# Kernel optimization log

Hardware: AMD Instinct MI355X
Metric: run time of the kernel (lower is better)

## Reference

```python
import jax, jax.numpy as jnp
import numpy as np

T, B, NIN, NOUT, H, NLAYER = 512, 32, 72, 90, 512, 5


def _ln(x, g, b):
    m = jnp.mean(x, -1, keepdims=True)
    v = jnp.var(x, -1, keepdims=True)
    return (x - m) * jax.lax.rsqrt(v + 1e-5) * g + b


def _sru_dir(xt, fp, rp, hw, vf, vr, bf, br):
    # xt/fp/rp/hw: (T, B, H) in scan order; elementwise gated recurrence
    def step(c, inp):
        x_t, f_t, r_t, hw_t = inp
        f = jax.nn.sigmoid(f_t + vf * c + bf)
        r = jax.nn.sigmoid(r_t + vr * c + br)
        c2 = f * c + (1.0 - f) * x_t
        h = r * jnp.tanh(c2) + (1.0 - r) * hw_t
        return c2, h
    c0 = jnp.zeros_like(xt[0])
    cT, hs = jax.lax.scan(step, c0, (xt, fp, rp, hw))
    return hs, cT


def _sru_layer(x, W, v, b, g, be, k):
    # x: (T, B, d_in); W: (d_in, 2*k*H); v,b: (2 dirs, 2 gates, H)
    Tl, Bl = x.shape[0], x.shape[1]
    xn = _ln(x, g, be)
    U = (xn @ W).reshape(Tl, Bl, 2, k, H)
    outs, cs = [], []
    for d in range(2):
        Ud = U[:, :, d]
        if d == 1:
            Ud = jnp.flip(Ud, 0)
        # highway: extra projection when d_in != H (k=4), else raw input (k=3)
        hw = Ud[:, :, 3] if k == 4 else (jnp.flip(x, 0) if d == 1 else x)
        hs, cT = _sru_dir(Ud[:, :, 0], Ud[:, :, 1], Ud[:, :, 2], hw,
                          v[d, 0], v[d, 1], b[d, 0], b[d, 1])
        if d == 1:
            hs = jnp.flip(hs, 0)
        outs.append(hs)
        cs.append(cT)
    return jnp.concatenate(outs, -1), jnp.concatenate(cs, -1)


def setup_inputs() -> dict:
    key = jax.random.key(0)
    ks = jax.random.split(key, 12)
    s1 = 1.0 / np.sqrt(NIN)
    s2 = 1.0 / np.sqrt(2 * H)
    s0 = 1.0 / np.sqrt(H)
    return {
        "x": jax.random.normal(ks[0], (T, B, NIN), jnp.float32),
        "W1": jax.random.normal(ks[1], (NIN, H), jnp.float32) * s1,
        "b1": jnp.zeros((H,), jnp.float32),
        "W2": jax.random.normal(ks[2], (2 * H, NOUT), jnp.float32) * s2,
        "b2": jnp.zeros((NOUT,), jnp.float32),
        # SRU layer 0: input H -> 2 dirs * H, k=3 (highway uses raw input)
        "W0": jax.random.normal(ks[3], (H, 2 * 3 * H), jnp.float32) * s0,
        "v0": jax.random.normal(ks[4], (2, 2, H), jnp.float32) * s0,
        "bb0": jnp.zeros((2, 2, H), jnp.float32),
        "g0": jnp.ones((H,), jnp.float32),
        "be0": jnp.zeros((H,), jnp.float32),
        # SRU layers 1..4: input 2H -> 2 dirs * H, k=4 (projected highway)
        "Ws": jax.random.normal(ks[5], (NLAYER - 1, 2 * H, 2 * 4 * H), jnp.float32) * s2,
        "vs": jax.random.normal(ks[6], (NLAYER - 1, 2, 2, H), jnp.float32) * s0,
        "bbs": jnp.zeros((NLAYER - 1, 2, 2, H), jnp.float32),
        "gs": jnp.ones((NLAYER - 1, 2 * H), jnp.float32),
        "bes": jnp.zeros((NLAYER - 1, 2 * H), jnp.float32),
    }


def reference(x, W1, b1, W2, b2, W0, v0, bb0, g0, be0, Ws, vs, bbs, gs, bes):
    h = jax.nn.relu(x @ W1 + b1)  # (T, B, H); dropout is identity at eval
    states = []
    h, c = _sru_layer(h, W0, v0, bb0, g0, be0, 3)
    states.append(c)
    for i in range(Ws.shape[0]):
        h, c = _sru_layer(h, Ws[i], vs[i], bbs[i], gs[i], bes[i], 4)
        states.append(c)
    out = h @ W2 + b2  # (T, B, NOUT)
    return out, jnp.stack(states)  # h state: (NLAYER, B, 2H)
```

## Files before the change

kernel.cpp:

```cpp
#include <hip/hip_runtime.h>
#include <stdint.h>

#define T_LEN 512
#define BATCH 32
#define NIN   72
#define NOUT  90
#define HDIM  512
#define MROWS (T_LEN*BATCH)

typedef unsigned short u16;
typedef unsigned int   u32;

typedef __bf16 bf16x8 __attribute__((ext_vector_type(8)));
typedef short  s16x8  __attribute__((ext_vector_type(8)));
typedef float  f32x4  __attribute__((ext_vector_type(4)));

__device__ __forceinline__ float b2f(u16 u){ return __uint_as_float(((u32)u)<<16); }
__device__ __forceinline__ u16 f2b(float x){
  u32 u = __float_as_uint(x);
  u += 0x7FFFu + ((u>>16)&1u);
  return (u16)(u>>16);
}
__device__ __forceinline__ float sigmoidf_(float z){ return 1.f/(1.f+__expf(-z)); }
__device__ __forceinline__ float tanhf_(float z){ return 2.f/(1.f+__expf(-2.f*z)) - 1.f; }

__device__ __forceinline__ void gload16(const void* g, void* l){
  __builtin_amdgcn_global_load_lds(
      (const __attribute__((address_space(1))) void*)g,
      (__attribute__((address_space(3))) void*)l, 16, 0, 0);
}

__global__ __launch_bounds__(256) void k_transpose_cast(
    const float* __restrict__ S, u16* __restrict__ D, int K, int N, int ldd)
{
  __shared__ float t[32][33];
  int k0 = blockIdx.y*32, n0 = blockIdx.x*32;
  int tx = threadIdx.x, ty = threadIdx.y;
  #pragma unroll
  for (int i=0;i<4;++i){
    int k = k0 + ty + i*8, n = n0 + tx;
    if (k < K && n < N) t[ty+i*8][tx] = S[(size_t)k*N + n];
  }
  __syncthreads();
  #pragma unroll
  for (int i=0;i<4;++i){
    int n = n0 + ty + i*8, k = k0 + tx;
    if (n < N && k < K) D[(size_t)n*ldd + k] = f2b(t[tx][ty+i*8]);
  }
}

__global__ __launch_bounds__(256) void k_gemm1_relu(
    const float* __restrict__ X, const float* __restrict__ W1,
    const float* __restrict__ b1, u16* __restrict__ H0)
{
  __shared__ float As[64][73];
  __shared__ float Bs[72][64];
  int m0 = blockIdx.y*64, n0 = blockIdx.x*64;
  int tid = threadIdx.x;
  for (int idx=tid; idx<64*NIN; idx+=256){ int r=idx/NIN, k=idx-r*NIN; As[r][k] = X[(size_t)(m0+r)*NIN + k]; }
  for (int idx=tid; idx<NIN*64; idx+=256){ int k=idx>>6, n=idx&63; Bs[k][n] = W1[(size_t)k*HDIM + n0+n]; }
  __syncthreads();
  int tx = tid & 15, ty = tid >> 4;
  float acc[4][4] = {};
  for (int k=0;k<NIN;++k){
    float a[4], bv[4];
    #pragma unroll
    for (int i=0;i<4;++i) a[i]=As[ty*4+i][k];
    #pragma unroll
    for (int j=0;j<4;++j) bv[j]=Bs[k][tx*4+j];
    #pragma unroll
    for (int i=0;i<4;++i)
      #pragma unroll
      for (int j=0;j<4;++j) acc[i][j] += a[i]*bv[j];
  }
  #pragma unroll
  for (int i=0;i<4;++i){
    int row = m0 + ty*4 + i;
    #pragma unroll
    for (int j=0;j<4;++j){
      int col = n0 + tx*4 + j;
      float v = acc[i][j] + b1[col];
      H0[(size_t)row*HDIM + col] = f2b(v > 0.f ? v : 0.f);
    }
  }
}

template<int D>
__global__ __launch_bounds__(256) void k_ln(
    const u16* __restrict__ X, const float* __restrict__ g,
    const float* __restrict__ be, u16* __restrict__ Y)
{
  int wrow = (blockIdx.x*256 + threadIdx.x) >> 6;
  int lane = threadIdx.x & 63;
  constexpr int E = D/64;
  const u16* row = X + (size_t)wrow*D;
  float vals[E];
  float s=0.f, s2=0.f;
  #pragma unroll
  for (int i=0;i<E/4;++i){
    ushort4 u = *(const ushort4*)(row + i*256 + lane*4);
    float v0=b2f(u.x), v1=b2f(u.y), v2=b2f(u.z), v3=b2f(u.w);
    vals[i*4+0]=v0; vals[i*4+1]=v1; vals[i*4+2]=v2; vals[i*4+3]=v3;
    s  += v0+v1+v2+v3;
    s2 += v0*v0+v1*v1+v2*v2+v3*v3;
  }
  #pragma unroll
  for (int off=32; off; off>>=1){ s += __shfl_xor(s,off); s2 += __shfl_xor(s2,off); }
  float mean = s * (1.f/D);
  float var  = s2 * (1.f/D) - mean*mean;
  float rstd = rsqrtf(var + 1e-5f);
  u16* yr = Y + (size_t)wrow*D;
  #pragma unroll
  for (int i=0;i<E/4;++i){
    int col = i*256 + lane*4;
    float4 gg = *(const float4*)(g+col);
    float4 bb = *(const float4*)(be+col);
    ushort4 o;
    o.x = f2b((vals[i*4+0]-mean)*rstd*gg.x + bb.x);
    o.y = f2b((vals[i*4+1]-mean)*rstd*gg.y + bb.y);
    o.z = f2b((vals[i*4+2]-mean)*rstd*gg.z + bb.z);
    o.w = f2b((vals[i*4+3]-mean)*rstd*gg.w + bb.w);
    *(ushort4*)(yr + col) = o;
  }
}

__global__ __launch_bounds__(512, 2) void k_gemm256(
    const u16* __restrict__ A, const u16* __restrict__ BT,
    u16* __restrict__ C, int K, int N)
{
  __shared__ u16 lds[65536];
  const int tid  = threadIdx.x;
  const int lane = tid & 63;
  const int wid  = tid >> 6;
  const int wm   = wid >> 2;
  const int wn   = wid & 3;

  const int nbx = gridDim.x;
  const int nwg = nbx * gridDim.y;
  const int bid = blockIdx.y * nbx + blockIdx.x;
  const int cpx = nwg >> 3;
  const int swz = (bid & 7) * cpx + (bid >> 3);
  const int m0 = (swz / nbx) * 256;
  const int n0 = (swz % nbx) * 256;

  const int l3 = lane >> 3, l7 = lane & 7;
  const int kswz = (l7 ^ l3) * 8;

  auto stageA = [&](int ts, int h, int db){
    const u16* base = A + (size_t)(m0 + h*128 + wid*8 + l3)*K + ts*64 + kswz;
    u16* dst = lds + db*32768 + h*8192 + wid*512;
    gload16(base,               dst);
    gload16(base + (size_t)64*K, dst + 4096);
  };
  auto stageB = [&](int ts, int db){
    const u16* base = BT + (size_t)(n0 + wid*8 + l3)*K + ts*64 + kswz;
    u16* dst = lds + db*32768 + 16384 + wid*512;
    gload16(base,                dst);
    gload16(base + (size_t) 64*K, dst + 4096);
    gload16(base + (size_t)128*K, dst + 8192);
    gload16(base + (size_t)192*K, dst + 12288);
  };
  auto rdfrag = [&](const u16* buf, int row, int ks)->bf16x8 {
    int byte = (row*128 + (ks*32 + ((lane>>4)*8))*2) ^ ((row&7)<<4);
    return __builtin_bit_cast(bf16x8, *(const s16x8*)((const char*)buf + byte));
  };

  f32x4 acc[8][4] = {};
  bf16x8 afr[2][2][2];
  bf16x8 bfr0[4][2], bfr1[4][2];
  const int nt = K >> 6;

  stageA(0, 0, 0);
  stageA(0, 1, 0);
  stageB(0, 0);
  asm volatile("s_waitcnt vmcnt(0)" ::: "memory");
  __builtin_amdgcn_sched_barrier(0);
  __builtin_amdgcn_s_barrier();
  __builtin_amdgcn_sched_barrier(0);
  #pragma unroll
  for (int n=0;n<4;++n)
    #pragma unroll
    for (int ks=0;ks<2;++ks)
      bfr0[n][ks] = rdfrag(lds + 16384, wn*64 + n*16 + (lane&15), ks);
  #pragma unroll
  for (int mm=0;mm<2;++mm)
    #pragma unroll
    for (int ks=0;ks<2;++ks)
      afr[0][mm][ks] = rdfrag(lds, wm*128 + mm*16 + (lane&15), ks);

  auto tile = [&](int t, bf16x8 (&bcur)[4][2], bf16x8 (&bnxt)[4][2]){
    const u16* bufA  = lds + (t & 1)*32768;
    const int  tn    = (t+1 < nt) ? t+1 : t;
    const int  db    = (t+1) & 1;
    const u16* bufAn = lds + db*32768;
    const u16* bufBn = bufAn + 16384;

    stageA(tn, 0, db);
    stageA(tn, 1, db);
    stageB(tn, db);

    #pragma unroll
    for (int q=0;q<3;++q){
      asm volatile("s_waitcnt lgkmcnt(0)" ::: "memory");
      __builtin_amdgcn_sched_barrier(0);
      #pragma unroll
      for (int mm=0;mm<2;++mm)
        #pragma unroll
        for (int ks=0;ks<2;++ks)
          afr[(q+1)&1][mm][ks] = rdfrag(bufA, wm*128 + ((q+1)*2+mm)*16 + (lane&15), ks);
      __builtin_amdgcn_sched_barrier(0);
      __builtin_amdgcn_s_setprio(1);
      #pragma unroll
      for (int mm=0;mm<2;++mm)
        #pragma unroll
        for (int n=0;n<4;++n)
          #pragma unroll
          for (int ks=0;ks<2;++ks)
            acc[q*2+mm][n] = __builtin_amdgcn_mfma_f32_16x16x32_bf16(
                afr[q&1][mm][ks], bcur[n][ks], acc[q*2+mm][n], 0,0,0);
      __builtin_amdgcn_s_setprio(0);
    }

    asm volatile("s_waitcnt vmcnt(0) lgkmcnt(0)" ::: "memory");
    __builtin_amdgcn_sched_barrier(0);
    __builtin_amdgcn_s_barrier();
    __builtin_amdgcn_sched_barrier(0);
    #pragma unroll
    for (int mm=0;mm<2;++mm)
      #pragma unroll
      for (int ks=0;ks<2;++ks)
        afr[0][mm][ks] = rdfrag(bufAn, wm*128 + mm*16 + (lane&15), ks);
    #pragma unroll
    for (int n=0;n<4;++n)
      #pragma unroll
      for (int ks=0;ks<2;++ks)
        bnxt[n][ks] = rdfrag(bufBn, wn*64 + n*16 + (lane&15), ks);
    __builtin_amdgcn_sched_barrier(0);
    __builtin_amdgcn_s_setprio(1);
    #pragma unroll
    for (int mm=0;mm<2;++mm)
      #pragma unroll
      for (int n=0;n<4;++n)
        #pragma unroll
        for (int ks=0;ks<2;++ks)
          acc[6+mm][n] = __builtin_amdgcn_mfma_f32_16x16x32_bf16(
              afr[1][mm][ks], bcur[n][ks], acc[6+mm][n], 0,0,0);
    __builtin_amdgcn_s_setprio(0);
  };

  for (int t = 0; t < nt; t += 2){
    tile(t,   bfr0, bfr1);
    tile(t+1, bfr1, bfr0);
  }

  #pragma unroll
  for (int m=0;m<8;++m){
    int row = m0 + wm*128 + m*16 + ((lane>>4)<<2);
    #pragma unroll
    for (int n=0;n<4;++n){
      int col = n0 + wn*64 + n*16 + (lane&15);
      #pragma unroll
      for (int i=0;i<4;++i)
        C[(size_t)(row+i)*N + col] = f2b(acc[m][n][i]);
    }
  }
}

template<bool OUT_F32, bool HAS_BIAS>
__global__ __launch_bounds__(256) void k_gemm(
    const u16* __restrict__ A, const u16* __restrict__ BT,
    void* __restrict__ Cv, const float* __restrict__ bias,
    int K, int N, int ldc, int nbound)
{
  __shared__ u16 As[128*64];
  __shared__ u16 Bs[128*64];
  const int tid  = threadIdx.x;
  const int lane = tid & 63;
  const int wid  = tid >> 6;

  const int nbx = gridDim.x;
  const int nwg = nbx * gridDim.y;
  const int bid = blockIdx.y * nbx + blockIdx.x;
  const int cpx = nwg >> 3;
  const int swzb = (bid & 7) * cpx + (bid >> 3);
  const int bx = swzb % nbx, by = swzb / nbx;

  const int m0 = by * 128;
  const int n0 = bx * 128;
  const int wr = wid >> 1, wc = wid & 1;
  f32x4 acc[4][4] = {};

  const int srow = lane >> 3;
  const int skel = (lane & 7) * 8;

  for (int kt = 0; kt < K; kt += 64) {
    #pragma unroll
    for (int i=0;i<4;++i){
      int seg  = wid*4 + i;
      int arow = seg*8 + srow;
      gload16(A  + (size_t)(m0 + arow)*K + kt + skel, As + seg*512);
      gload16(BT + (size_t)(n0 + arow)*K + kt + skel, Bs + seg*512);
    }
    __syncthreads();
    #pragma unroll
    for (int ks=0; ks<2; ++ks){
      bf16x8 a[4], b[4];
      #pragma unroll
      for (int m=0;m<4;++m){
        int off = (wr*64 + m*16 + (lane&15))*64 + ks*32 + (lane>>4)*8;
        a[m] = __builtin_bit_cast(bf16x8, *(const s16x8*)(As + off));
      }
      #pragma unroll
      for (int n=0;n<4;++n){
        int off = (wc*64 + n*16 + (lane&15))*64 + ks*32 + (lane>>4)*8;
        b[n] = __builtin_bit_cast(bf16x8, *(const s16x8*)(Bs + off));
      }
      #pragma unroll
      for (int m=0;m<4;++m)
        #pragma unroll
        for (int n=0;n<4;++n)
          acc[m][n] = __builtin_amdgcn_mfma_f32_16x16x32_bf16(a[m], b[n], acc[m][n], 0,0,0);
    }
    __syncthreads();
  }

  #pragma unroll
  for (int m=0;m<4;++m){
    #pragma unroll
    for (int n=0;n<4;++n){
      int col = n0 + wc*64 + n*16 + (lane & 15);
      #pragma unroll
      for (int i=0;i<4;++i){
        int row = m0 + wr*64 + m*16 + ((lane>>4)<<2) + i;
        float v = acc[m][n][i];
        if (OUT_F32) {
          if (col < nbound){
            float bv = HAS_BIAS ? bias[col] : 0.f;
            ((float*)Cv)[(size_t)row*ldc + col] = v + bv;
          }
        } else {
          ((u16*)Cv)[(size_t)row*ldc + col] = f2b(v);
        }
      }
    }
  }
}

template<int KG>
__global__ __launch_bounds__(64) void k_scan(
    const u16* __restrict__ U, const u16* __restrict__ hwsrc,
    const float* __restrict__ v, const float* __restrict__ bb,
    u16* __restrict__ hout, float* __restrict__ states)
{
  constexpr int NS = 4;
  constexpr int D  = 3;
  constexpr int NI = T_LEN/8;
  __shared__ u16 ring[NS*2048];

  const int lane = threadIdx.x;
  const int bid  = blockIdx.x;
  const int hblk = bid & 7;
  const int b    = (bid >> 3) & 31;
  const int d    = bid >> 8;
  const int h    = hblk*64 + lane;
  const int RS   = 2*KG*HDIM;

  const int s2 = lane >> 5, p = (lane>>3)&3, c7 = lane&7;

  auto issue = [&](int k, int slot){
    #pragma unroll
    for (int half=0; half<4; ++half){
      int s = 8*k + 2*half + s2;
      int t = d ? (T_LEN-1-s) : s;
      int row = t*BATCH + b;
      const u16* g;
      if (KG == 4 || p < 3)
        g = U + (size_t)row*RS + (size_t)(d*KG + p)*HDIM + hblk*64 + c7*8;
      else
        g = hwsrc + (size_t)row*HDIM + hblk*64 + c7*8;
      gload16(g, &ring[slot*2048 + half*512]);
    }
  };
  auto ldslot = [&](int k, float (&xq)[8], float (&fq)[8], float (&rq)[8], float (&wq)[8]){
    const u16* base = ring + (k & (NS-1))*2048;
    #pragma unroll
    for (int j=0;j<8;++j){
      xq[j] = b2f(base[j*256 + 0*64 + lane]);
      fq[j] = b2f(base[j*256 + 1*64 + lane]);
      rq[j] = b2f(base[j*256 + 2*64 + lane]);
      wq[j] = b2f(base[j*256 + 3*64 + lane]);
    }
  };

  for (int k=0;k<D;++k) issue(k, k);
  asm volatile("s_waitcnt vmcnt(0)" ::: "memory");
  __builtin_amdgcn_sched_barrier(0);

  const float vf  = v[(d*2+0)*HDIM + h];
  const float vr  = v[(d*2+1)*HDIM + h];
  const float bf_ = bb[(d*2+0)*HDIM + h];
  const float br_ = bb[(d*2+1)*HDIM + h];

  float xA[8], fA[8], rA[8], wA[8];
  float xB[8], fB[8], rB[8], wB[8];
  ldslot(0, xA, fA, rA, wA);
  asm volatile("s_waitcnt lgkmcnt(0)" ::: "memory");
  __builtin_amdgcn_sched_barrier(0);

  float cst = 0.f;
  auto compute8 = [&](int k, float (&xq)[8], float (&fq)[8], float (&rq)[8], float (&wq)[8]){
    #pragma unroll
    for (int j=0;j<8;++j){
      int s = 8*k + j;
      int t = d ? (T_LEN-1-s) : s;
      float f = sigmoidf_(fq[j] + vf*cst + bf_);
      float r = sigmoidf_(rq[j] + vr*cst + br_);
      cst = xq[j] + f*(cst - xq[j]);
      float hv = wq[j] + r*(tanhf_(cst) - wq[j]);
      hout[(size_t)(t*BATCH + b)*(2*HDIM) + d*HDIM + h] = f2b(hv);
    }
  };

  for (int k=0; k<NI; k+=2){
    {
      int kk = (k+D < NI) ? (k+D) : (NI-1);
      issue(kk, (k+D) & (NS-1));
      asm volatile("s_waitcnt vmcnt(24)" ::: "memory");
      __builtin_amdgcn_sched_barrier(0);
      ldslot(k+1, xB, fB, rB, wB);
      __builtin_amdgcn_sched_barrier(0);
      compute8(k, xA, fA, rA, wA);
      asm volatile("s_waitcnt lgkmcnt(0)" ::: "memory");
      __builtin_amdgcn_sched_barrier(0);
    }
    {
      int kk = (k+1+D < NI) ? (k+1+D) : (NI-1);
      issue(kk, (k+1+D) & (NS-1));
      asm volatile("s_waitcnt vmcnt(24)" ::: "memory");
      __builtin_amdgcn_sched_barrier(0);
      if (k+2 < NI) ldslot(k+2, xA, fA, rA, wA);
      __builtin_amdgcn_sched_barrier(0);
      compute8(k+1, xB, fB, rB, wB);
      asm volatile("s_waitcnt lgkmcnt(0)" ::: "memory");
      __builtin_amdgcn_sched_barrier(0);
    }
  }
  states[(size_t)b*(2*HDIM) + d*HDIM + h] = cst;
}

extern "C" void kernel_launch(void* const* d_in, const int* in_sizes, int n_in,
                              void* d_out, int out_size, void* d_ws, size_t ws_size,
                              hipStream_t stream)
{
  const float* x   = (const float*)d_in[0];
  const float* W1  = (const float*)d_in[1];
  const float* b1  = (const float*)d_in[2];
  const float* W2  = (const float*)d_in[3];
  const float* b2  = (const float*)d_in[4];
  const float* W0  = (const float*)d_in[5];
  const float* v0  = (const float*)d_in[6];
  const float* bb0 = (const float*)d_in[7];
  const float* g0  = (const float*)d_in[8];
  const float* be0 = (const float*)d_in[9];
  const float* Ws  = (const float*)d_in[10];
  const float* vs  = (const float*)d_in[11];
  const float* bbs = (const float*)d_in[12];
  const float* gs  = (const float*)d_in[13];
  const float* bes = (const float*)d_in[14];
  (void)in_sizes; (void)n_in; (void)out_size; (void)ws_size;

  char* ws = (char*)d_ws;
  size_t off = 0;
  auto alloc = [&](size_t bytes)->void*{
    void* p = ws + off; off += (bytes + 255) & ~(size_t)255; return p;
  };
  u16* W0T  = (u16*)alloc((size_t)3072*512*2);
  u16* WsT  = (u16*)alloc((size_t)4*4096*1024*2);
  u16* W2T  = (u16*)alloc((size_t)128*1024*2);
  u16* h0   = (u16*)alloc((size_t)MROWS*512*2);
  u16* xn   = (u16*)alloc((size_t)MROWS*1024*2);
  u16* Ubuf = (u16*)alloc((size_t)MROWS*4096*2);
  u16* hbuf = (u16*)alloc((size_t)MROWS*1024*2);

  float* outp   = (float*)d_out;
  float* states = outp + (size_t)MROWS*NOUT;

  hipMemsetAsync(W2T, 0, (size_t)128*1024*2, stream);
  k_transpose_cast<<<dim3(3072/32, 512/32), dim3(32,8), 0, stream>>>(W0, W0T, 512, 3072, 512);
  for (int i=0;i<4;++i)
    k_transpose_cast<<<dim3(4096/32, 1024/32), dim3(32,8), 0, stream>>>(
        Ws + (size_t)i*1024*4096, WsT + (size_t)i*4096*1024, 1024, 4096, 1024);
  k_transpose_cast<<<dim3(3, 1024/32), dim3(32,8), 0, stream>>>(W2, W2T, 1024, NOUT, 1024);

  k_gemm1_relu<<<dim3(HDIM/64, MROWS/64), 256, 0, stream>>>(x, W1, b1, h0);

  k_ln<512><<<MROWS/4, 256, 0, stream>>>(h0, g0, be0, xn);
  k_gemm256<<<dim3(3072/256, MROWS/256), 512, 0, stream>>>(xn, W0T, Ubuf, 512, 3072);
  k_scan<3><<<512, 64, 0, stream>>>(Ubuf, h0, v0, bb0, hbuf, states);

  for (int i=0;i<4;++i){
    k_ln<1024><<<MROWS/4, 256, 0, stream>>>(hbuf, gs + (size_t)i*1024, bes + (size_t)i*1024, xn);
    k_gemm256<<<dim3(4096/256, MROWS/256), 512, 0, stream>>>(
        xn, WsT + (size_t)i*4096*1024, Ubuf, 1024, 4096);
    k_scan<4><<<512, 64, 0, stream>>>(Ubuf, nullptr, vs + (size_t)i*2048, bbs + (size_t)i*2048,
                                      hbuf, states + (size_t)(i+1)*BATCH*1024);
  }

  k_gemm<true,true><<<dim3(1, MROWS/128), 256, 0, stream>>>(
      hbuf, W2T, d_out, b2, 1024, 128, NOUT, NOUT);
}
```

Baseline: 1.211 ms.

## Restructure 256x256 GEMM to 16 waves with BK=32 and smaller per-wave tiles

The big projection GEMM now runs 1024 threads (16 waves) per block, each wave computing a 64x64 sub-tile instead of 128x64. The K step shrinks from 64 to 32, so LDS drops to 64 KB, and a new XOR swizzle is used for the global-to-LDS loads and the fragment reads. The aim is more waves in flight and fewer registers per wave to hide latency. In exchange there are twice as many K iterations and barriers, and fewer MFMAs run between each sync.

Measured after the change: 1.238 ms. +2.2%, slower.

```diff
diff --git a/kernel.cpp b/kernel.cpp
--- a/kernel.cpp
+++ b/kernel.cpp
@@ -124,11 +124,11 @@
   }
 }
 
-__global__ __launch_bounds__(512, 2) void k_gemm256(
+__global__ __launch_bounds__(1024, 1) void k_gemm256(
     const u16* __restrict__ A, const u16* __restrict__ BT,
     u16* __restrict__ C, int K, int N)
 {
-  __shared__ u16 lds[65536];
+  __shared__ u16 lds[32768];
   const int tid  = threadIdx.x;
   const int lane = tid & 63;
   const int wid  = tid >> 6;
@@ -143,35 +143,30 @@
   const int m0 = (swz / nbx) * 256;
   const int n0 = (swz % nbx) * 256;
 
-  const int l3 = lane >> 3, l7 = lane & 7;
-  const int kswz = (l7 ^ l3) * 8;
-
-  auto stageA = [&](int ts, int h, int db){
-    const u16* base = A + (size_t)(m0 + h*128 + wid*8 + l3)*K + ts*64 + kswz;
-    u16* dst = lds + db*32768 + h*8192 + wid*512;
-    gload16(base,               dst);
-    gload16(base + (size_t)64*K, dst + 4096);
+  const int glog = lane ^ ((lane >> 3) & 7);
+  const int srow = glog >> 2;
+  const int sq   = glog & 3;
+
+  auto stageA = [&](int ts, int db){
+    gload16(A + (size_t)(m0 + wid*16 + srow)*K + ts*32 + sq*8,
+            lds + db*16384 + wid*512);
   };
   auto stageB = [&](int ts, int db){
-    const u16* base = BT + (size_t)(n0 + wid*8 + l3)*K + ts*64 + kswz;
-    u16* dst = lds + db*32768 + 16384 + wid*512;
-    gload16(base,                dst);
-    gload16(base + (size_t) 64*K, dst + 4096);
-    gload16(base + (size_t)128*K, dst + 8192);
-    gload16(base + (size_t)192*K, dst + 12288);
-  };
-  auto rdfrag = [&](const u16* buf, int row, int ks)->bf16x8 {
-    int byte = (row*128 + (ks*32 + ((lane>>4)*8))*2) ^ ((row&7)<<4);
-    return __builtin_bit_cast(bf16x8, *(const s16x8*)((const char*)buf + byte));
-  };
-
-  f32x4 acc[8][4] = {};
-  bf16x8 afr[2][2][2];
-  bf16x8 bfr0[4][2], bfr1[4][2];
-  const int nt = K >> 6;
-
-  stageA(0, 0, 0);
-  stageA(0, 1, 0);
+    gload16(BT + (size_t)(n0 + wid*16 + srow)*K + ts*32 + sq*8,
+            lds + db*16384 + 8192 + wid*512);
+  };
+  auto rdfrag = [&](const u16* buf, int row)->bf16x8 {
+    int gr = row*4 + (lane>>4);
+    gr ^= (gr>>3)&7;
+    return __builtin_bit_cast(bf16x8, *(const s16x8*)((const char*)buf + gr*16));
+  };
+
+  f32x4 acc[4][4] = {};
+  bf16x8 afr[2];
+  bf16x8 bfr[4];
+  const int nt = K >> 5;
+
+  stageA(0, 0);
   stageB(0, 0);
   asm volatile("s_waitcnt vmcnt(0)" ::: "memory");
   __builtin_amdgcn_sched_barrier(0);
@@ -179,83 +174,47 @@
   __builtin_amdgcn_sched_barrier(0);
   #pragma unroll
   for (int n=0;n<4;++n)
-    #pragma unroll
-    for (int ks=0;ks<2;++ks)
-      bfr0[n][ks] = rdfrag(lds + 16384, wn*64 + n*16 + (lane&15), ks);
-  #pragma unroll
-  for (int mm=0;mm<2;++mm)
-    #pragma unroll
-    for (int ks=0;ks<2;++ks)
-      afr[0][mm][ks] = rdfrag(lds, wm*128 + mm*16 + (lane&15), ks);
-
-  auto tile = [&](int t, bf16x8 (&bcur)[4][2], bf16x8 (&bnxt)[4][2]){
-    const u16* bufA  = lds + (t & 1)*32768;
-    const int  tn    = (t+1 < nt) ? t+1 : t;
-    const int  db    = (t+1) & 1;
-    const u16* bufAn = lds + db*32768;
-    const u16* bufBn = bufAn + 16384;
-
-    stageA(tn, 0, db);
-    stageA(tn, 1, db);
+    bfr[n] = rdfrag(lds + 8192, wn*64 + n*16 + (lane&15));
+  afr[0] = rdfrag(lds, wm*64 + (lane&15));
+
+  for (int t = 0; t < nt; ++t){
+    const u16* bufA = lds + (t & 1)*16384;
+    const int  tn   = (t+1 < nt) ? t+1 : t;
+    const int  db   = (t+1) & 1;
+    const u16* bufAn = lds + db*16384;
+    const u16* bufBn = bufAn + 8192;
+
+    stageA(tn, db);
     stageB(tn, db);
 
     #pragma unroll
-    for (int q=0;q<3;++q){
+    for (int q=0;q<4;++q){
       asm volatile("s_waitcnt lgkmcnt(0)" ::: "memory");
       __builtin_amdgcn_sched_barrier(0);
-      #pragma unroll
-      for (int mm=0;mm<2;++mm)
-        #pragma unroll
-        for (int ks=0;ks<2;++ks)
-          afr[(q+1)&1][mm][ks] = rdfrag(bufA, wm*128 + ((q+1)*2+mm)*16 + (lane&15), ks);
+      if (q < 3)
+        afr[(q+1)&1] = rdfrag(bufA, wm*64 + (q+1)*16 + (lane&15));
       __builtin_amdgcn_sched_barrier(0);
       __builtin_amdgcn_s_setprio(1);
       #pragma unroll
-      for (int mm=0;mm<2;++mm)
-        #pragma unroll
-        for (int n=0;n<4;++n)
-          #pragma unroll
-          for (int ks=0;ks<2;++ks)
-            acc[q*2+mm][n] = __builtin_amdgcn_mfma_f32_16x16x32_bf16(
-                afr[q&1][mm][ks], bcur[n][ks], acc[q*2+mm][n], 0,0,0);
+      for (int n=0;n<4;++n)
+        acc[q][n] = __builtin_amdgcn_mfma_f32_16x16x32_bf16(
+            afr[q&1], bfr[n], acc[q][n], 0,0,0);
       __builtin_amdgcn_s_setprio(0);
     }
 
-    asm volatile("s_waitcnt vmcnt(0) lgkmcnt(0)" ::: "memory");
+    asm volatile("s_waitcnt vmcnt(0)" ::: "memory");
     __builtin_amdgcn_sched_barrier(0);
     __builtin_amdgcn_s_barrier();
     __builtin_amdgcn_sched_barrier(0);
     #pragma unroll
-    for (int mm=0;mm<2;++mm)
-      #pragma unroll
-      for (int ks=0;ks<2;++ks)
-        afr[0][mm][ks] = rdfrag(bufAn, wm*128 + mm*16 + (lane&15), ks);
-    #pragma unroll
     for (int n=0;n<4;++n)
-      #pragma unroll
-      for (int ks=0;ks<2;++ks)
-        bnxt[n][ks] = rdfrag(bufBn, wn*64 + n*16 + (lane&15), ks);
-    __builtin_amdgcn_sched_barrier(0);
-    __builtin_amdgcn_s_setprio(1);
-    #pragma unroll
-    for (int mm=0;mm<2;++mm)
-      #pragma unroll
-      for (int n=0;n<4;++n)
-        #pragma unroll
-        for (int ks=0;ks<2;++ks)
-          acc[6+mm][n] = __builtin_amdgcn_mfma_f32_16x16x32_bf16(
-              afr[1][mm][ks], bcur[n][ks], acc[6+mm][n], 0,0,0);
-    __builtin_amdgcn_s_setprio(0);
-  };
-
-  for (int t = 0; t < nt; t += 2){
-    tile(t,   bfr0, bfr1);
-    tile(t+1, bfr1, bfr0);
-  }
-
-  #pragma unroll
-  for (int m=0;m<8;++m){
-    int row = m0 + wm*128 + m*16 + ((lane>>4)<<2);
+      bfr[n] = rdfrag(bufBn, wn*64 + n*16 + (lane&15));
+    afr[0] = rdfrag(bufAn, wm*64 + (lane&15));
+  }
+
+  #pragma unroll
+  for (int m=0;m<4;++m){
+    int row = m0 + wm*64 + m*16 + ((lane>>4)<<2);
     #pragma unroll
     for (int n=0;n<4;++n){
       int col = n0 + wn*64 + n*16 + (lane&15);
@@ -495,12 +454,12 @@
   k_gemm1_relu<<<dim3(HDIM/64, MROWS/64), 256, 0, stream>>>(x, W1, b1, h0);
 
   k_ln<512><<<MROWS/4, 256, 0, stream>>>(h0, g0, be0, xn);
-  k_gemm256<<<dim3(3072/256, MROWS/256), 512, 0, stream>>>(xn, W0T, Ubuf, 512, 3072);
+  k_gemm256<<<dim3(3072/256, MROWS/256), 1024, 0, stream>>>(xn, W0T, Ubuf, 512, 3072);
   k_scan<3><<<512, 64, 0, stream>>>(Ubuf, h0, v0, bb0, hbuf, states);
 
   for (int i=0;i<4;++i){
     k_ln<1024><<<MROWS/4, 256, 0, stream>>>(hbuf, gs + (size_t)i*1024, bes + (size_t)i*1024, xn);
-    k_gemm256<<<dim3(4096/256, MROWS/256), 512, 0, stream>>>(
+    k_gemm256<<<dim3(4096/256, MROWS/256), 1024, 0, stream>>>(
         xn, WsT + (size_t)i*4096*1024, Ubuf, 1024, 4096);
     k_scan<4><<<512, 64, 0, stream>>>(Ubuf, nullptr, vs + (size_t)i*2048, bbs + (size_t)i*2048,
                                       hbuf, states + (size_t)(i+1)*BATCH*1024);
```
